# Performance work log

Hardware: AMD Instinct MI355X
Metric: run time of the kernel (lower is better)

The kernel has to match this reference:

```python
import jax, jax.numpy as jnp
import numpy as np

NODE_DIM, HIDDEN_DIM, OUT_DIM = 64, 128, 64
N_NODES, N_EDGES = 50000, 800000
SLOPE = 0.05


def leaky(x):
    return jnp.where(x >= 0, x, SLOPE * x)


def setup_inputs() -> dict:
    key = jax.random.key(0)
    ks = jax.random.split(key, 8)
    x = jax.random.normal(ks[0], (N_NODES, NODE_DIM), dtype=jnp.float32)
    edge_index = jax.random.randint(ks[1], (2, N_EDGES), 0, N_NODES, dtype=jnp.int64)
    s0 = 1.0 / np.sqrt(NODE_DIM)
    s1 = 1.0 / np.sqrt(HIDDEN_DIM)
    W0 = jax.random.uniform(ks[2], (NODE_DIM, HIDDEN_DIM), jnp.float32, -s0, s0)
    b0 = jax.random.uniform(ks[3], (HIDDEN_DIM,), jnp.float32, -s0, s0)
    W1 = jax.random.uniform(ks[4], (HIDDEN_DIM, HIDDEN_DIM), jnp.float32, -s1, s1)
    b1 = jax.random.uniform(ks[5], (HIDDEN_DIM,), jnp.float32, -s1, s1)
    W2 = jax.random.uniform(ks[6], (HIDDEN_DIM, OUT_DIM), jnp.float32, -s1, s1)
    b2 = jax.random.uniform(ks[7], (OUT_DIM,), jnp.float32, -s1, s1)
    return {"x": x, "edge_index": edge_index, "W0": W0, "b0": b0,
            "W1": W1, "b1": b1, "W2": W2, "b2": b2}


def reference(x, edge_index, W0, b0, W1, b1, W2, b2):
    # gather-sum: [E, node_dim]
    e = x[edge_index[0]] + x[edge_index[1]]
    h = leaky(e @ W0 + b0)          # [E, hidden]
    h = leaky(h @ W1 + b1)          # [E, hidden]
    out = leaky(h @ W2 + b2)        # [E, out]
    return out
```

## Files before the change

### kernel.cpp

```cpp
#include <hip/hip_runtime.h>

typedef _Float16 half8  __attribute__((ext_vector_type(8)));
typedef float    floatx4 __attribute__((ext_vector_type(4)));

#define N_NODES 50000
#define N_EDGES 800000
#define SLOPE 0.05f

#define WS_XH  0ull
#define WS_WC  (WS_XH + (size_t)N_NODES * 64 * 2)
#define WS_B0  (WS_WC + 65536)
#define WS_B1  (WS_B0 + 512)
#define WS_B2  (WS_B1 + 512)

#define HC_STRIDE 40
#define XCONV_BLOCKS 782
#define PREP_BLOCKS (XCONV_BLOCKS + 65)

__device__ __forceinline__ float leaky(float t) { return t >= 0.f ? t : SLOPE * t; }

__device__ __forceinline__ void load_lds16(const void* g, void* l) {
    __builtin_amdgcn_global_load_lds(
        (const __attribute__((address_space(1))) void*)g,
        (__attribute__((address_space(3))) void*)l, 16, 0, 0);
}

__global__ void prep_kernel(const float* __restrict__ x,
                            const float* __restrict__ W0, const float* __restrict__ W1,
                            const float* __restrict__ W2, const float* __restrict__ b0,
                            const float* __restrict__ b1, const float* __restrict__ b2,
                            unsigned char* __restrict__ ws) {
    const int b = blockIdx.x;
    if (b < XCONV_BLOCKS) {
        _Float16* xh = (_Float16*)(ws + WS_XH);
        const int i = (b * 512 + threadIdx.x) * 8;
        if (i < N_NODES * 64) {
            floatx4 u0 = *(const floatx4*)(x + i);
            floatx4 u1 = *(const floatx4*)(x + i + 4);
            half8 h;
            #pragma unroll
            for (int j = 0; j < 4; ++j) { h[j] = (_Float16)u0[j]; h[4 + j] = (_Float16)u1[j]; }
            *(half8*)(xh + i) = h;
        }
        return;
    }
    const int t = (b - XCONV_BLOCKS) * 512 + threadIdx.x;
    _Float16* wc = (_Float16*)(ws + WS_WC);
    if (t < 16384) {
        int k = t >> 7, n = t & 127;
        wc[n * 128 + (k ^ ((n & 7) << 3))] = (_Float16)W1[k * 128 + n];
    } else if (t < 24576) {
        int i2 = t - 16384, k = i2 >> 6, n = i2 & 63;
        wc[16384 + n * 128 + (k ^ ((n & 7) << 3))] = (_Float16)W2[k * 64 + n];
    } else if (t < 32768) {
        int i2 = t - 24576, n = i2 >> 6, k = i2 & 63;
        wc[24576 + n * 64 + (k ^ ((n & 7) << 3))] = (_Float16)W0[k * 128 + n];
    } else if (t < 33088) {
        int i2 = t - 32768;
        if (i2 < 128) ((float*)(ws + WS_B0))[i2] = b0[i2];
        else if (i2 < 256) ((float*)(ws + WS_B1))[i2 - 128] = b1[i2 - 128];
        else ((float*)(ws + WS_B2))[i2 - 256] = b2[i2 - 256];
    }
}

__global__ __launch_bounds__(512, 4) void edge_kernel(const int* __restrict__ ei,
                                                      const unsigned char* __restrict__ ws,
                                                      float* __restrict__ out) {
    __shared__ __align__(16) _Float16 wlds[32768];
    __shared__ __align__(16) _Float16 hc[8][16 * HC_STRIDE];
    __shared__ __align__(16) float b0s[128], b1s[128], b2s[64];

    const _Float16* __restrict__ xh = (const _Float16*)(ws + WS_XH);
    const _Float16* __restrict__ w1s = wlds;
    const _Float16* __restrict__ w2s = wlds + 16384;
    const _Float16* __restrict__ w0s = wlds + 24576;

    const int wave = threadIdx.x >> 6, lane = threadIdx.x & 63;
    const int cl = lane & 15, q = lane >> 4;
    const int base = blockIdx.x * 256 + wave * 32;

    const int r0 = base + cl;
    const int s0 = ei[r0], d0 = ei[N_EDGES + r0];
    const int s1 = ei[r0 + 16], d1 = ei[N_EDGES + r0 + 16];

    const _Float16* ps0 = xh + (size_t)s0 * 64 + q * 8;
    const _Float16* pd0 = xh + (size_t)d0 * 64 + q * 8;
    const _Float16* ps1 = xh + (size_t)s1 * 64 + q * 8;
    const _Float16* pd1 = xh + (size_t)d1 * 64 + q * 8;
    half8 us00 = *(const half8*)(ps0);  half8 us01 = *(const half8*)(ps0 + 32);
    half8 ud00 = *(const half8*)(pd0);  half8 ud01 = *(const half8*)(pd0 + 32);
    half8 us10 = *(const half8*)(ps1);  half8 us11 = *(const half8*)(ps1 + 32);
    half8 ud10 = *(const half8*)(pd1);  half8 ud11 = *(const half8*)(pd1 + 32);

    {
        const char* wcg = (const char*)(ws + WS_WC);
        #pragma unroll
        for (int it = 0; it < 8; ++it) {
            const int c = wave * 8 + it;
            load_lds16(wcg + c * 1024 + lane * 16, (char*)wlds + c * 1024);
        }
        const int t = threadIdx.x;
        if (t < 128) { b0s[t] = *(const float*)(ws + WS_B0 + t * 4);
                       b1s[t] = *(const float*)(ws + WS_B1 + t * 4); }
        else if (t < 192) b2s[t - 128] = *(const float*)(ws + WS_B2 + (size_t)(t - 128) * 4);
    }
    __syncthreads();

    half8 a0[2][2];
    a0[0][0] = us00 + ud00;  a0[0][1] = us01 + ud01;
    a0[1][0] = us10 + ud10;  a0[1][1] = us11 + ud11;

    const int swz = (cl & 7) << 3;
    _Float16* hw = &hc[wave][0];

    half8 a1[2][4];
    #pragma unroll
    for (int kk = 0; kk < 4; ++kk) {
        const int nA = 2 * kk, nB = 2 * kk + 1;
        half8 wA0 = *(const half8*)&w0s[((nA * 16 + cl) * 64 + q * 8) ^ swz];
        half8 wA1 = *(const half8*)&w0s[((nA * 16 + cl) * 64 + 32 + q * 8) ^ swz];
        half8 wB0 = *(const half8*)&w0s[((nB * 16 + cl) * 64 + q * 8) ^ swz];
        half8 wB1 = *(const half8*)&w0s[((nB * 16 + cl) * 64 + 32 + q * 8) ^ swz];
        const float bbA = b0s[nA * 16 + cl], bbB = b0s[nB * 16 + cl];
        #pragma unroll
        for (int g = 0; g < 2; ++g) {
            floatx4 cA = {0.f, 0.f, 0.f, 0.f}, cB = {0.f, 0.f, 0.f, 0.f};
            cA = __builtin_amdgcn_mfma_f32_16x16x32_f16(a0[g][0], wA0, cA, 0, 0, 0);
            cA = __builtin_amdgcn_mfma_f32_16x16x32_f16(a0[g][1], wA1, cA, 0, 0, 0);
            cB = __builtin_amdgcn_mfma_f32_16x16x32_f16(a0[g][0], wB0, cB, 0, 0, 0);
            cB = __builtin_amdgcn_mfma_f32_16x16x32_f16(a0[g][1], wB1, cB, 0, 0, 0);
            #pragma unroll
            for (int rr = 0; rr < 4; ++rr) {
                hw[(q * 4 + rr) * HC_STRIDE + cl]      = (_Float16)leaky(cA[rr] + bbA);
                hw[(q * 4 + rr) * HC_STRIDE + 16 + cl] = (_Float16)leaky(cB[rr] + bbB);
            }
            a1[g][kk] = *(const half8*)&hw[cl * HC_STRIDE + q * 8];
        }
    }

    floatx4 acc2[2][4];
    #pragma unroll
    for (int g = 0; g < 2; ++g)
        #pragma unroll
        for (int n2 = 0; n2 < 4; ++n2) acc2[g][n2] = (floatx4){0.f, 0.f, 0.f, 0.f};

    #pragma unroll
    for (int ks = 0; ks < 4; ++ks) {
        const int nA = 2 * ks, nB = 2 * ks + 1;
        floatx4 cA0 = {0.f,0.f,0.f,0.f}, cA1 = {0.f,0.f,0.f,0.f};
        floatx4 cB0 = {0.f,0.f,0.f,0.f}, cB1 = {0.f,0.f,0.f,0.f};
        #pragma unroll
        for (int kk = 0; kk < 4; ++kk) {
            half8 b = *(const half8*)&w1s[((nA * 16 + cl) * 128 + kk * 32 + q * 8) ^ swz];
            cA0 = __builtin_amdgcn_mfma_f32_16x16x32_f16(a1[0][kk], b, cA0, 0, 0, 0);
            cA1 = __builtin_amdgcn_mfma_f32_16x16x32_f16(a1[1][kk], b, cA1, 0, 0, 0);
        }
        #pragma unroll
        for (int kk = 0; kk < 4; ++kk) {
            half8 b = *(const half8*)&w1s[((nB * 16 + cl) * 128 + kk * 32 + q * 8) ^ swz];
            cB0 = __builtin_amdgcn_mfma_f32_16x16x32_f16(a1[0][kk], b, cB0, 0, 0, 0);
            cB1 = __builtin_amdgcn_mfma_f32_16x16x32_f16(a1[1][kk], b, cB1, 0, 0, 0);
        }
        const float bbA = b1s[nA * 16 + cl], bbB = b1s[nB * 16 + cl];
        half8 a2[2];
        #pragma unroll
        for (int g = 0; g < 2; ++g) {
            const floatx4 cc0 = g ? cA1 : cA0;
            const floatx4 cc1 = g ? cB1 : cB0;
            #pragma unroll
            for (int rr = 0; rr < 4; ++rr) {
                hw[(q * 4 + rr) * HC_STRIDE + cl]      = (_Float16)leaky(cc0[rr] + bbA);
                hw[(q * 4 + rr) * HC_STRIDE + 16 + cl] = (_Float16)leaky(cc1[rr] + bbB);
            }
            a2[g] = *(const half8*)&hw[cl * HC_STRIDE + q * 8];
        }
        #pragma unroll
        for (int n2 = 0; n2 < 4; ++n2) {
            half8 b = *(const half8*)&w2s[((n2 * 16 + cl) * 128 + ks * 32 + q * 8) ^ swz];
            acc2[0][n2] = __builtin_amdgcn_mfma_f32_16x16x32_f16(b, a2[0], acc2[0][n2], 0, 0, 0);
            acc2[1][n2] = __builtin_amdgcn_mfma_f32_16x16x32_f16(b, a2[1], acc2[1][n2], 0, 0, 0);
        }
    }

    #pragma unroll
    for (int n2 = 0; n2 < 4; ++n2) {
        floatx4 bb = *(const floatx4*)&b2s[n2 * 16 + q * 4];
        #pragma unroll
        for (int g = 0; g < 2; ++g) {
            floatx4 o;
            #pragma unroll
            for (int rr = 0; rr < 4; ++rr) o[rr] = leaky(acc2[g][n2][rr] + bb[rr]);
            *(floatx4*)(out + (size_t)(base + g * 16 + cl) * 64 + n2 * 16 + q * 4) = o;
        }
    }
}

extern "C" void kernel_launch(void* const* d_in, const int* in_sizes, int n_in,
                              void* d_out, int out_size, void* d_ws, size_t ws_size,
                              hipStream_t stream) {
    const float* x  = (const float*)d_in[0];
    const int*   ei = (const int*)d_in[1];
    const float* W0 = (const float*)d_in[2];
    const float* b0 = (const float*)d_in[3];
    const float* W1 = (const float*)d_in[4];
    const float* b1 = (const float*)d_in[5];
    const float* W2 = (const float*)d_in[6];
    const float* b2 = (const float*)d_in[7];
    float* out = (float*)d_out;
    unsigned char* ws = (unsigned char*)d_ws;

    prep_kernel<<<PREP_BLOCKS, 512, 0, stream>>>(x, W0, W1, W2, b0, b1, b2, ws);
    edge_kernel<<<N_EDGES / 256, 512, 0, stream>>>(ei, ws, out);
}
```

Baseline: 286.4 us.

## Fold biases into MFMA accumulators, swizzle staging LDS, add setprio, plain weight copy

Initializes MFMA accumulators with the bias values so the separate bias add disappears from each epilogue. XOR-swizzles the per-wave LDS staging writes and reads to cut bank conflicts, and wraps MFMA groups in s_setprio to favour matrix issue. The weight preload switches from direct global-to-LDS loads to a plain register-mediated copy, and the output store loop order is swapped. The copy change may add register pressure and latency during the prologue.

Result: faster. 277.4 us (-3.2%).

```diff
diff --git a/kernel.cpp b/kernel.cpp
--- a/kernel.cpp
+++ b/kernel.cpp
@@ -18,12 +18,6 @@
 #define PREP_BLOCKS (XCONV_BLOCKS + 65)
 
 __device__ __forceinline__ float leaky(float t) { return t >= 0.f ? t : SLOPE * t; }
-
-__device__ __forceinline__ void load_lds16(const void* g, void* l) {
-    __builtin_amdgcn_global_load_lds(
-        (const __attribute__((address_space(1))) void*)g,
-        (__attribute__((address_space(3))) void*)l, 16, 0, 0);
-}
 
 __global__ void prep_kernel(const float* __restrict__ x,
                             const float* __restrict__ W0, const float* __restrict__ W1,
@@ -93,11 +87,12 @@
     half8 ud10 = *(const half8*)(pd1);  half8 ud11 = *(const half8*)(pd1 + 32);
 
     {
-        const char* wcg = (const char*)(ws + WS_WC);
+        const half8* __restrict__ wcg = (const half8*)(ws + WS_WC);
+        half8* wl = (half8*)wlds;
         #pragma unroll
         for (int it = 0; it < 8; ++it) {
-            const int c = wave * 8 + it;
-            load_lds16(wcg + c * 1024 + lane * 16, (char*)wlds + c * 1024);
+            const int c = threadIdx.x + it * 512;
+            wl[c] = wcg[c];
         }
         const int t = threadIdx.x;
         if (t < 128) { b0s[t] = *(const float*)(ws + WS_B0 + t * 4);
@@ -111,7 +106,9 @@
     a0[1][0] = us10 + ud10;  a0[1][1] = us11 + ud11;
 
     const int swz = (cl & 7) << 3;
+    const int wxor = (q & 2) << 3;
     _Float16* hw = &hc[wave][0];
+    const int hrd = cl * HC_STRIDE + ((q * 8) ^ ((cl & 8) << 1));
 
     half8 a1[2][4];
     #pragma unroll
@@ -124,31 +121,37 @@
         const float bbA = b0s[nA * 16 + cl], bbB = b0s[nB * 16 + cl];
         #pragma unroll
         for (int g = 0; g < 2; ++g) {
-            floatx4 cA = {0.f, 0.f, 0.f, 0.f}, cB = {0.f, 0.f, 0.f, 0.f};
+            floatx4 cA = {bbA, bbA, bbA, bbA};
+            floatx4 cB = {bbB, bbB, bbB, bbB};
+            __builtin_amdgcn_s_setprio(1);
             cA = __builtin_amdgcn_mfma_f32_16x16x32_f16(a0[g][0], wA0, cA, 0, 0, 0);
             cA = __builtin_amdgcn_mfma_f32_16x16x32_f16(a0[g][1], wA1, cA, 0, 0, 0);
             cB = __builtin_amdgcn_mfma_f32_16x16x32_f16(a0[g][0], wB0, cB, 0, 0, 0);
             cB = __builtin_amdgcn_mfma_f32_16x16x32_f16(a0[g][1], wB1, cB, 0, 0, 0);
+            __builtin_amdgcn_s_setprio(0);
             #pragma unroll
             for (int rr = 0; rr < 4; ++rr) {
-                hw[(q * 4 + rr) * HC_STRIDE + cl]      = (_Float16)leaky(cA[rr] + bbA);
-                hw[(q * 4 + rr) * HC_STRIDE + 16 + cl] = (_Float16)leaky(cB[rr] + bbB);
+                hw[(q * 4 + rr) * HC_STRIDE + (cl ^ wxor)]        = (_Float16)leaky(cA[rr]);
+                hw[(q * 4 + rr) * HC_STRIDE + ((16 + cl) ^ wxor)] = (_Float16)leaky(cB[rr]);
             }
-            a1[g][kk] = *(const half8*)&hw[cl * HC_STRIDE + q * 8];
+            a1[g][kk] = *(const half8*)&hw[hrd];
         }
     }
 
     floatx4 acc2[2][4];
     #pragma unroll
-    for (int g = 0; g < 2; ++g)
-        #pragma unroll
-        for (int n2 = 0; n2 < 4; ++n2) acc2[g][n2] = (floatx4){0.f, 0.f, 0.f, 0.f};
+    for (int n2 = 0; n2 < 4; ++n2) {
+        const floatx4 bb2 = *(const floatx4*)&b2s[n2 * 16 + q * 4];
+        acc2[0][n2] = bb2;  acc2[1][n2] = bb2;
+    }
 
     #pragma unroll
     for (int ks = 0; ks < 4; ++ks) {
         const int nA = 2 * ks, nB = 2 * ks + 1;
-        floatx4 cA0 = {0.f,0.f,0.f,0.f}, cA1 = {0.f,0.f,0.f,0.f};
-        floatx4 cB0 = {0.f,0.f,0.f,0.f}, cB1 = {0.f,0.f,0.f,0.f};
+        const float bbA = b1s[nA * 16 + cl], bbB = b1s[nB * 16 + cl];
+        floatx4 cA0 = {bbA,bbA,bbA,bbA}, cA1 = {bbA,bbA,bbA,bbA};
+        floatx4 cB0 = {bbB,bbB,bbB,bbB}, cB1 = {bbB,bbB,bbB,bbB};
+        __builtin_amdgcn_s_setprio(1);
         #pragma unroll
         for (int kk = 0; kk < 4; ++kk) {
             half8 b = *(const half8*)&w1s[((nA * 16 + cl) * 128 + kk * 32 + q * 8) ^ swz];
@@ -161,7 +164,7 @@
             cB0 = __builtin_amdgcn_mfma_f32_16x16x32_f16(a1[0][kk], b, cB0, 0, 0, 0);
             cB1 = __builtin_amdgcn_mfma_f32_16x16x32_f16(a1[1][kk], b, cB1, 0, 0, 0);
         }
-        const float bbA = b1s[nA * 16 + cl], bbB = b1s[nB * 16 + cl];
+        __builtin_amdgcn_s_setprio(0);
         half8 a2[2];
         #pragma unroll
         for (int g = 0; g < 2; ++g) {
@@ -169,27 +172,28 @@
             const floatx4 cc1 = g ? cB1 : cB0;
             #pragma unroll
             for (int rr = 0; rr < 4; ++rr) {
-                hw[(q * 4 + rr) * HC_STRIDE + cl]      = (_Float16)leaky(cc0[rr] + bbA);
-                hw[(q * 4 + rr) * HC_STRIDE + 16 + cl] = (_Float16)leaky(cc1[rr] + bbB);
+                hw[(q * 4 + rr) * HC_STRIDE + (cl ^ wxor)]        = (_Float16)leaky(cc0[rr]);
+                hw[(q * 4 + rr) * HC_STRIDE + ((16 + cl) ^ wxor)] = (_Float16)leaky(cc1[rr]);
             }
-            a2[g] = *(const half8*)&hw[cl * HC_STRIDE + q * 8];
-        }
+            a2[g] = *(const half8*)&hw[hrd];
+        }
+        __builtin_amdgcn_s_setprio(1);
         #pragma unroll
         for (int n2 = 0; n2 < 4; ++n2) {
             half8 b = *(const half8*)&w2s[((n2 * 16 + cl) * 128 + ks * 32 + q * 8) ^ swz];
             acc2[0][n2] = __builtin_amdgcn_mfma_f32_16x16x32_f16(b, a2[0], acc2[0][n2], 0, 0, 0);
             acc2[1][n2] = __builtin_amdgcn_mfma_f32_16x16x32_f16(b, a2[1], acc2[1][n2], 0, 0, 0);
         }
-    }
-
-    #pragma unroll
-    for (int n2 = 0; n2 < 4; ++n2) {
-        floatx4 bb = *(const floatx4*)&b2s[n2 * 16 + q * 4];
-        #pragma unroll
-        for (int g = 0; g < 2; ++g) {
+        __builtin_amdgcn_s_setprio(0);
+    }
+
+    #pragma unroll
+    for (int g = 0; g < 2; ++g) {
+        #pragma unroll
+        for (int n2 = 0; n2 < 4; ++n2) {
             floatx4 o;
             #pragma unroll
-            for (int rr = 0; rr < 4; ++rr) o[rr] = leaky(acc2[g][n2][rr] + bb[rr]);
+            for (int rr = 0; rr < 4; ++rr) o[rr] = leaky(acc2[g][n2][rr]);
             *(floatx4*)(out + (size_t)(base + g * 16 + cl) * 64 + n2 * 16 + q * 4) = o;
         }
     }
```
